# Kernel tuning notes

Measured on AMD Instinct MI355X. Metric: run time of the kernel, lower is better.

## Reference

```python
import jax, jax.numpy as jnp
import numpy as np

N_HEADS = 16
N_KV_HEADS = 4
HEAD_DIM = 128
D_MODEL = 2048
WINDOW = 1024
THETA = 10000.0
EPS = 1e-6


def _rmsnorm(x, w):
    var = jnp.mean(x * x, axis=-1, keepdims=True)
    return x * jax.lax.rsqrt(var + EPS) * w


def _rope(x, pos):
    # x: [B, H, S, D]; rotate-half (llama-style) RoPE
    d2 = HEAD_DIM // 2
    inv_freq = 1.0 / (THETA ** (jnp.arange(0, HEAD_DIM, 2, dtype=jnp.float32) / HEAD_DIM))
    ang = pos[:, None].astype(jnp.float32) * inv_freq[None, :]  # [S, D/2]
    cos = jnp.cos(ang)[None, None]
    sin = jnp.sin(ang)[None, None]
    x1, x2 = x[..., :d2], x[..., d2:]
    return jnp.concatenate([x1 * cos - x2 * sin, x1 * sin + x2 * cos], axis=-1)


def setup_inputs() -> dict:
    key = jax.random.key(0)
    ks = jax.random.split(key, 7)
    B, S = 1, 2048
    s = 0.02
    return {
        "x": jax.random.normal(ks[0], (B, S, D_MODEL), jnp.float32),
        "wq": jax.random.normal(ks[1], (N_HEADS * HEAD_DIM, D_MODEL), jnp.float32) * s,
        "wk": jax.random.normal(ks[2], (N_KV_HEADS * HEAD_DIM, D_MODEL), jnp.float32) * s,
        "wv": jax.random.normal(ks[3], (N_KV_HEADS * HEAD_DIM, D_MODEL), jnp.float32) * s,
        "wo": jax.random.normal(ks[4], (D_MODEL, N_HEADS * HEAD_DIM), jnp.float32) * s,
        "q_norm_w": jnp.ones((HEAD_DIM,), jnp.float32),
        "k_norm_w": jnp.ones((HEAD_DIM,), jnp.float32),
    }


def reference(x, wq, wk, wv, wo, q_norm_w, k_norm_w):
    B, S, _ = x.shape
    past_length = 0
    scale = HEAD_DIM ** -0.5
    n_rep = N_HEADS // N_KV_HEADS

    q = (x @ wq.T).reshape(B, S, N_HEADS, HEAD_DIM).transpose(0, 2, 1, 3)
    k = (x @ wk.T).reshape(B, S, N_KV_HEADS, HEAD_DIM).transpose(0, 2, 1, 3)
    v = (x @ wv.T).reshape(B, S, N_KV_HEADS, HEAD_DIM).transpose(0, 2, 1, 3)

    q = _rmsnorm(q, q_norm_w)
    k = _rmsnorm(k, k_norm_w)

    pos = jnp.arange(S) + past_length
    q = _rope(q, pos)
    k = _rope(k, pos)

    # GQA: materialize repeated KV heads, as in _repeat_kv
    k_rep = jnp.repeat(k, n_rep, axis=1)  # [B, H, S, D]
    v_rep = jnp.repeat(v, n_rep, axis=1)

    # sliding-window causal mask (total_seq_len=S > WINDOW)
    q_idx = jnp.arange(S)[:, None] + past_length
    k_idx = jnp.arange(S)[None, :]
    mask = (q_idx >= k_idx) & (q_idx - k_idx < WINDOW)  # [S, S]

    scores = jnp.einsum("bhqd,bhkd->bhqk", q, k_rep) * scale
    scores = jnp.where(mask[None, None], scores, jnp.float32(-jnp.inf))
    attn = jax.nn.softmax(scores, axis=-1)
    out = jnp.einsum("bhqk,bhkd->bhqd", attn, v_rep)

    out = out.transpose(0, 2, 1, 3).reshape(B, S, N_HEADS * HEAD_DIM)
    return out @ wo.T
```

## Files before the change

kernel.cpp:

```cpp
#include <hip/hip_runtime.h>
#include <hip/hip_bf16.h>
#include <cstdint>
#include <cstddef>

typedef __attribute__((ext_vector_type(4))) float f32x4;
typedef __attribute__((ext_vector_type(8))) short bf16x8;
typedef __attribute__((ext_vector_type(8))) unsigned short us8;

#define MFMA16(a, b, c) __builtin_amdgcn_mfma_f32_16x16x32_bf16(a, b, c, 0, 0, 0)

__device__ inline unsigned short f2bf(float f) {
    unsigned int u = __float_as_uint(f);
    u += 0x7fffu + ((u >> 16) & 1u);
    return (unsigned short)(u >> 16);
}
__device__ inline float bf2f(unsigned short u) {
    return __uint_as_float((unsigned int)u << 16);
}
__device__ inline unsigned short f2bf_fast(float f) {
    float r;
    asm("v_cvt_pk_bf16_f32 %0, %1, %2" : "=v"(r) : "v"(f), "v"(f));
    return (unsigned short)__float_as_uint(r);
}

__device__ inline void gload_lds16(const void* g, void* l) {
    __builtin_amdgcn_global_load_lds(
        (const __attribute__((address_space(1))) void*)g,
        (__attribute__((address_space(3))) void*)l, 16, 0, 0);
}
__device__ inline unsigned lds_addr(const void* p) {
    return (unsigned)(size_t)((__attribute__((address_space(3))) const void*)p);
}

__global__ __launch_bounds__(256) void prep_all(const float* __restrict__ x,
                                                const float* __restrict__ wq,
                                                const float* __restrict__ wk,
                                                const float* __restrict__ wv,
                                                const float* __restrict__ wo,
                                                unsigned short* __restrict__ xb,
                                                unsigned short* __restrict__ wqkv,
                                                unsigned short* __restrict__ wob,
                                                float2* __restrict__ tbl) {
    const int b = blockIdx.x;
    if (b < 14336) {
        const float* src; unsigned short* dst; int off4;
        if (b < 4096)       { src = x;  dst = xb;                 off4 = b; }
        else if (b < 8192)  { src = wq; dst = wqkv;               off4 = b - 4096; }
        else if (b < 9216)  { src = wk; dst = wqkv + 2048 * 2048; off4 = b - 8192; }
        else if (b < 10240) { src = wv; dst = wqkv + 2560 * 2048; off4 = b - 9216; }
        else                { src = wo; dst = wob;                off4 = b - 10240; }
        int i = (off4 * 256 + threadIdx.x) * 4;
        float4 v = *(const float4*)(src + i);
        ushort4 o;
        o.x = f2bf(v.x); o.y = f2bf(v.y); o.z = f2bf(v.z); o.w = f2bf(v.w);
        *(ushort4*)(dst + i) = o;
    } else {
        int idx = (b - 14336) * 256 + threadIdx.x;
        int row = idx >> 6, t = idx & 63;
        float inv_freq = exp2f((float)t * (-2.0f / 128.0f) * 13.287712379549449f);
        float s, c;
        sincosf((float)row * inv_freq, &s, &c);
        tbl[idx] = make_float2(c, s);
    }
}

__global__ __launch_bounds__(512, 2) void gemm256(const unsigned short* __restrict__ A,
                                                  const unsigned short* __restrict__ B,
                                                  unsigned short* __restrict__ Cp,
                                                  int M, int N, int Kfull, int kspan) {
    __shared__ unsigned short As[3][8192];
    __shared__ unsigned short Bs[3][8192];
    const int tid = threadIdx.x;
    const int lane = tid & 63, wave = tid >> 6;
    const int wr = wave >> 2, wc = wave & 3;
    const int l15 = lane & 15, l4 = lane >> 4;
    const int gx = gridDim.x;
    const int nwg = gx * gridDim.y;
    const int bid0 = blockIdx.y * gx + blockIdx.x;
    const int q8 = nwg >> 3, r8 = nwg & 7;
    const int xcd = bid0 & 7, sub = bid0 >> 3;
    const int wgid = ((xcd < r8) ? xcd * (q8 + 1) : r8 * (q8 + 1) + (xcd - r8) * q8) + sub;
    const int bm = wgid / gx, bn = wgid % gx;
    const int z = blockIdx.z;
    const unsigned short* Az = A + (size_t)z * kspan;
    const unsigned short* Bz = B + (size_t)z * kspan;
    unsigned short* C = Cp + (size_t)z * M * N;
    const int nK = kspan >> 5;

    f32x4 acc[8][4] = {};

    const int r0 = tid >> 2, qs = tid & 3;
    const int qsw = qs ^ ((r0 >> 1) & 3);
    const unsigned short* pa0 = Az + (size_t)(bm * 256 + r0) * Kfull + qsw * 8;
    const unsigned short* pa1 = pa0 + (size_t)128 * Kfull;
    const unsigned short* pb0 = Bz + (size_t)(bn * 256 + r0) * Kfull + qsw * 8;
    const unsigned short* pb1 = pb0 + (size_t)128 * Kfull;

#define STG(kt, bb)                                            \
    do {                                                       \
        gload_lds16(pa0 + (kt) * 32, &As[bb][tid * 8]);        \
        gload_lds16(pa1 + (kt) * 32, &As[bb][4096 + tid * 8]); \
        gload_lds16(pb0 + (kt) * 32, &Bs[bb][tid * 8]);        \
        gload_lds16(pb1 + (kt) * 32, &Bs[bb][4096 + tid * 8]); \
    } while (0)

    const int q = l4 ^ ((l15 >> 1) & 3);
    const unsigned aB = lds_addr(&As[0][0]) + (unsigned)((wr * 128 + l15) * 64 + q * 16);
    const unsigned bB = lds_addr(&Bs[0][0]) + (unsigned)((wc * 64 + l15) * 64 + q * 16);

#define DSR(dst, addr, off) \
    asm volatile("ds_read_b128 %0, %1 offset:" #off : "=v"(dst) : "v"(addr))

    STG(0, 0);
    STG(1, 1);
    int bc = 0, bs = 2;
    for (int kt = 0; kt < nK; ++kt) {
        if (kt + 1 < nK)
            asm volatile("s_waitcnt vmcnt(4)\ns_barrier" ::: "memory");
        else
            asm volatile("s_waitcnt vmcnt(0)\ns_barrier" ::: "memory");
        __builtin_amdgcn_sched_barrier(0);

        bf16x8 a[8], b[4];
        {
            const unsigned aA = aB + bc * 16384;
            const unsigned bA = bB + bc * 16384;
            DSR(a[0], aA, 0);    DSR(a[1], aA, 1024);
            DSR(a[2], aA, 2048); DSR(a[3], aA, 3072);
            DSR(a[4], aA, 4096); DSR(a[5], aA, 5120);
            DSR(a[6], aA, 6144); DSR(a[7], aA, 7168);
            DSR(b[0], bA, 0);    DSR(b[1], bA, 1024);
            DSR(b[2], bA, 2048); DSR(b[3], bA, 3072);
        }
        if (kt + 2 < nK) STG(kt + 2, bs);
        asm volatile("s_waitcnt lgkmcnt(0)" ::: "memory");
        __builtin_amdgcn_sched_barrier(0);

        __builtin_amdgcn_s_setprio(1);
#pragma unroll
        for (int m = 0; m < 8; ++m)
#pragma unroll
            for (int n = 0; n < 4; ++n)
                acc[m][n] = MFMA16(a[m], b[n], acc[m][n]);
        __builtin_amdgcn_s_setprio(0);

        if (++bc == 3) bc = 0;
        if (++bs == 3) bs = 0;
    }
#undef STG
#undef DSR

    for (int m = 0; m < 8; ++m)
        for (int n = 0; n < 4; ++n)
            for (int j = 0; j < 4; ++j) {
                int row = bm * 256 + wr * 128 + m * 16 + l4 * 4 + j;
                int col = bn * 256 + wc * 64 + n * 16 + l15;
                C[(size_t)row * N + col] = f2bf_fast(acc[m][n][j]);
            }
}

__global__ __launch_bounds__(256) void norm_rope(const unsigned short* __restrict__ p0,
                                                 const unsigned short* __restrict__ p1,
                                                 const float* __restrict__ qw,
                                                 const float* __restrict__ kw,
                                                 const float2* __restrict__ tbl,
                                                 unsigned short* __restrict__ Qb,
                                                 unsigned short* __restrict__ Kb) {
    const int row = blockIdx.x;
    const int head = blockIdx.y * 4 + (threadIdx.x >> 6);
    const int t = threadIdx.x & 63;
    const size_t off = (size_t)row * 3072 + head * 128;
    float x1 = bf2f(p0[off + t]) + bf2f(p1[off + t]);
    float x2 = bf2f(p0[off + t + 64]) + bf2f(p1[off + t + 64]);
    float ss = x1 * x1 + x2 * x2;
    for (int m = 32; m; m >>= 1) ss += __shfl_xor(ss, m);
    float r = rsqrtf(ss * (1.0f / 128.0f) + 1e-6f);
    const float* w = (head < 16) ? qw : kw;
    float y1 = x1 * r * w[t], y2 = x2 * r * w[t + 64];
    float2 cs = tbl[row * 64 + t];
    x1 = y1 * cs.x - y2 * cs.y;
    x2 = y1 * cs.y + y2 * cs.x;
    if (head < 16) {
        const float SCALE2 = 0.12751879526654698f;
        x1 *= SCALE2; x2 *= SCALE2;
    }
    unsigned short* dst = (head < 16) ? Qb + ((size_t)head * 2048 + row) * 128
                                      : Kb + ((size_t)(head - 16) * 2048 + row) * 128;
    dst[t] = f2bf(x1);
    dst[t + 64] = f2bf(x2);
}

__global__ __launch_bounds__(256) void transpose_v(const unsigned short* __restrict__ p0,
                                                   const unsigned short* __restrict__ p1,
                                                   unsigned short* __restrict__ VbT) {
    const int kt = blockIdx.x;
    const int h  = blockIdx.y;
    __shared__ unsigned short T[64 * 132];
    const int tid = threadIdx.x;
    for (int i = 0; i < 8; ++i) {
        int s = i * 256 + tid;
        int r = s >> 5, c = (s & 31) * 4;
        size_t off = (size_t)(kt * 64 + r) * 3072 + (20 + h) * 128 + c;
        ushort4 a = *(const ushort4*)(p0 + off);
        ushort4 b = *(const ushort4*)(p1 + off);
        ushort4 o;
        o.x = f2bf(bf2f(a.x) + bf2f(b.x));
        o.y = f2bf(bf2f(a.y) + bf2f(b.y));
        o.z = f2bf(bf2f(a.z) + bf2f(b.z));
        o.w = f2bf(bf2f(a.w) + bf2f(b.w));
        *(ushort4*)&T[r * 132 + c] = o;
    }
    __syncthreads();
    for (int i = 0; i < 4; ++i) {
        int s = i * 256 + tid;
        int d = s >> 3, ck = (s & 7) * 8;
        us8 v;
        for (int j = 0; j < 8; ++j) v[j] = T[(ck + j) * 132 + d];
        *(us8*)(VbT + (size_t)h * 128 * 2048 + (size_t)d * 2048 + kt * 64 + ck) = v;
    }
}

__global__ __launch_bounds__(256) void attn_fwd(const unsigned short* __restrict__ Qb,
                                                const unsigned short* __restrict__ Kb,
                                                const unsigned short* __restrict__ VbT,
                                                unsigned short* __restrict__ Ob) {
    const int bid = blockIdx.x;
    const int seq = bid >> 3;
    const int h = (bid & 7) * 2 + (seq >> 5);
    const int qt = seq & 31;
    const int kvh = h >> 2;
    const int q0 = qt * 64;
    __shared__ unsigned short Ks[2][64 * 128];
    __shared__ unsigned short Vs[128 * 64];
    __shared__ unsigned short Ps[4][16 * 72];
    const int tid = threadIdx.x;
    const int lane = tid & 63, wave = tid >> 6;
    const int l15 = lane & 15, l4 = lane >> 4;

    bf16x8 qf[4];
    {
        const unsigned short* qrow =
            Qb + ((size_t)h * 2048 + q0 + wave * 16 + l15) * 128 + l4 * 8;
        for (int kk = 0; kk < 4; ++kk) qf[kk] = *(const bf16x8*)(qrow + kk * 32);
    }
    f32x4 o[8] = {};
    float m2[4], lp[4];
    for (int j = 0; j < 4; ++j) { m2[j] = -1e30f; lp[j] = 0.0f; }
    const int kt_lo = (qt >= 16) ? (qt - 16) : 0;

    const unsigned short* Kh = Kb + (size_t)kvh * 2048 * 128;
    const unsigned short* Vh = VbT + (size_t)kvh * 128 * 2048;

    int ksr[4], ksc[4], vsr[4], vsc[4];
    for (int i = 0; i < 4; ++i) {
        int s = i * 256 + tid;
        ksr[i] = s >> 4;
        ksc[i] = (((s & 15) * 16) ^ ((ksr[i] & 7) << 4)) >> 1;
        vsr[i] = s >> 3;
        vsc[i] = (((s & 7) * 16) ^ ((vsr[i] & 7) << 4)) >> 1;
    }

    for (int i = 0; i < 4; ++i)
        gload_lds16(Kh + (size_t)(kt_lo * 64 + ksr[i]) * 128 + ksc[i], &Ks[0][(i * 256 + tid) * 8]);

    int cur = 0;
    for (int kt = kt_lo; kt <= qt; ++kt) {
        asm volatile("s_waitcnt vmcnt(0)\ns_barrier" ::: "memory");
        __builtin_amdgcn_sched_barrier(0);

        for (int i = 0; i < 4; ++i)
            gload_lds16(Vh + (size_t)vsr[i] * 2048 + kt * 64 + vsc[i], &Vs[(i * 256 + tid) * 8]);
        if (kt < qt) {
            for (int i = 0; i < 4; ++i)
                gload_lds16(Kh + (size_t)((kt + 1) * 64 + ksr[i]) * 128 + ksc[i],
                            &Ks[cur ^ 1][(i * 256 + tid) * 8]);
        }

        f32x4 s[4] = {};
        __builtin_amdgcn_s_setprio(1);
        for (int nn = 0; nn < 4; ++nn)
            for (int kk = 0; kk < 4; ++kk) {
                int r = nn * 16 + l15;
                int cb = (kk * 64 + l4 * 16) ^ ((r & 7) << 4);
                bf16x8 kf = *(const bf16x8*)((const char*)&Ks[cur][0] + r * 256 + cb);
                s[nn] = MFMA16(qf[kk], kf, s[nn]);
            }
        __builtin_amdgcn_s_setprio(0);

        float p[4][4];
        const bool masked = (kt == qt) || (qt >= 16 && kt == kt_lo);
        if (masked) {
            for (int nn = 0; nn < 4; ++nn) {
                int kc = kt * 64 + nn * 16 + l15;
                for (int j = 0; j < 4; ++j) {
                    int qr = q0 + wave * 16 + l4 * 4 + j;
                    unsigned diff = (unsigned)(qr - kc);
                    p[nn][j] = (diff < 1024u) ? s[nn][j] : -1e30f;
                }
            }
        } else {
            for (int nn = 0; nn < 4; ++nn)
                for (int j = 0; j < 4; ++j) p[nn][j] = s[nn][j];
        }

        float mxl[4];
        bool flag = true;
        for (int j = 0; j < 4; ++j) {
            mxl[j] = fmaxf(fmaxf(p[0][j], p[1][j]), fmaxf(p[2][j], p[3][j]));
            flag = flag && (mxl[j] <= m2[j] + 11.0f);
        }
        if (!__all(flag)) {
            for (int j = 0; j < 4; ++j) {
                float mx = mxl[j];
                for (int mk = 8; mk; mk >>= 1) mx = fmaxf(mx, __shfl_xor(mx, mk));
                float mnew = fmaxf(m2[j], mx);
                float corr = exp2f(m2[j] - mnew);
                m2[j] = mnew;
                lp[j] *= corr;
                for (int dd = 0; dd < 8; ++dd) o[dd][j] *= corr;
            }
        }
        for (int j = 0; j < 4; ++j) {
            float rs = 0.0f;
            for (int nn = 0; nn < 4; ++nn) {
                float pv = exp2f(p[nn][j] - m2[j]);
                p[nn][j] = pv;
                rs += pv;
            }
            lp[j] += rs;
        }

        for (int j = 0; j < 4; ++j)
            for (int nn = 0; nn < 4; ++nn)
                Ps[wave][(l4 * 4 + j) * 72 + nn * 16 + l15] = f2bf_fast(p[nn][j]);

        bf16x8 pa[2];
        for (int kk2 = 0; kk2 < 2; ++kk2)
            pa[kk2] = *(const bf16x8*)&Ps[wave][l15 * 72 + kk2 * 32 + l4 * 8];

        if (kt < qt)
            asm volatile("s_waitcnt vmcnt(4)\ns_barrier" ::: "memory");
        else
            asm volatile("s_waitcnt vmcnt(0)\ns_barrier" ::: "memory");
        __builtin_amdgcn_sched_barrier(0);

        __builtin_amdgcn_s_setprio(1);
        for (int dd = 0; dd < 8; ++dd)
            for (int kk2 = 0; kk2 < 2; ++kk2) {
                int d = dd * 16 + l15;
                int cb = (kk2 * 64 + l4 * 16) ^ ((d & 7) << 4);
                bf16x8 vf = *(const bf16x8*)((const char*)&Vs[0] + d * 128 + cb);
                o[dd] = MFMA16(pa[kk2], vf, o[dd]);
            }
        __builtin_amdgcn_s_setprio(0);
        cur ^= 1;
    }

    for (int j = 0; j < 4; ++j) {
        float lt = lp[j];
        for (int mk = 8; mk; mk >>= 1) lt += __shfl_xor(lt, mk);
        float inv = 1.0f / lt;
        int row = q0 + wave * 16 + l4 * 4 + j;
        unsigned short* orow = Ob + (size_t)row * 2048 + h * 128;
        for (int dd = 0; dd < 8; ++dd) orow[dd * 16 + l15] = f2bf_fast(o[dd][j] * inv);
    }
}

__global__ __launch_bounds__(256) void add4(const unsigned short* __restrict__ p,
                                            float* __restrict__ out, int n) {
    int i = (blockIdx.x * 256 + threadIdx.x) * 8;
    if (i >= n) return;
    us8 a = *(const us8*)(p + i);
    us8 b = *(const us8*)(p + 4194304 + i);
    us8 c = *(const us8*)(p + 8388608 + i);
    us8 d = *(const us8*)(p + 12582912 + i);
    f32x4 o0, o1;
    for (int j = 0; j < 4; ++j)
        o0[j] = (bf2f(a[j]) + bf2f(b[j])) + (bf2f(c[j]) + bf2f(d[j]));
    for (int j = 0; j < 4; ++j)
        o1[j] = (bf2f(a[j + 4]) + bf2f(b[j + 4])) + (bf2f(c[j + 4]) + bf2f(d[j + 4]));
    *(f32x4*)(out + i) = o0;
    *(f32x4*)(out + i + 4) = o1;
}

extern "C" void kernel_launch(void* const* d_in, const int* in_sizes, int n_in,
                              void* d_out, int out_size, void* d_ws, size_t ws_size,
                              hipStream_t stream) {
    const float* x  = (const float*)d_in[0];
    const float* wq = (const float*)d_in[1];
    const float* wk = (const float*)d_in[2];
    const float* wv = (const float*)d_in[3];
    const float* wo = (const float*)d_in[4];
    const float* wo_ = wo; (void)wo_;
    const float* qw = (const float*)d_in[5];
    const float* kw = (const float*)d_in[6];
    float* out = (float*)d_out;

    char* ws = (char*)d_ws;
    unsigned short* xb   = (unsigned short*)(ws + 0);
    unsigned short* wqkv = (unsigned short*)(ws + 8388608);
    unsigned short* wob  = (unsigned short*)(ws + 20971520);
    unsigned short* qkvP = (unsigned short*)(ws + 29360128);
    unsigned short* Qb   = (unsigned short*)(ws + 54525952);
    unsigned short* Kb   = (unsigned short*)(ws + 62914560);
    unsigned short* VbT  = (unsigned short*)(ws + 65011712);
    unsigned short* Ob   = (unsigned short*)(ws + 67108864);
    unsigned short* outP = (unsigned short*)(ws + 29360128);
    float2*         tbl  = (float2*)(ws + 104857600);

    prep_all<<<dim3(14848), dim3(256), 0, stream>>>(x, wq, wk, wv, wo, xb, wqkv, wob, tbl);
    gemm256<<<dim3(12, 8, 2), dim3(512), 0, stream>>>(xb, wqkv, qkvP, 2048, 3072, 2048, 1024);
    norm_rope<<<dim3(2048, 5), dim3(256), 0, stream>>>(qkvP, qkvP + 2048 * 3072, qw, kw, tbl, Qb, Kb);
    transpose_v<<<dim3(32, 4), dim3(256), 0, stream>>>(qkvP, qkvP + 2048 * 3072, VbT);
    attn_fwd<<<dim3(512), dim3(256), 0, stream>>>(Qb, Kb, VbT, Ob);
    gemm256<<<dim3(8, 8, 4), dim3(512), 0, stream>>>(Ob, wob, outP, 2048, 2048, 2048, 512);
    add4<<<dim3(2048), dim3(256), 0, stream>>>(outP, out, 2048 * 2048);
}
```

Before: 133.7 us.

## Share K/V tiles across two query heads per attention block

The attention kernel now launches 256 blocks of 512 threads. Each block covers two query heads that map to the same KV head, so each K/V tile loaded into LDS serves twice as many waves, halving global K/V traffic and per-head load instructions. The P tile is written as packed bf16 pairs into an XOR-swizzled LDS layout to reduce bank conflicts. To keep the P·V product correct, the V transpose kernel stores keys in a matching permuted order. Larger blocks reduce the number of resident blocks and leave the causal load imbalance between blocks unchanged.

Measured after the change: 126.5 us. -5.4%, faster.

```diff
diff --git a/kernel.cpp b/kernel.cpp
--- a/kernel.cpp
+++ b/kernel.cpp
@@ -215,32 +215,37 @@
         int s = i * 256 + tid;
         int d = s >> 3, ck = (s & 7) * 8;
         us8 v;
-        for (int j = 0; j < 8; ++j) v[j] = T[(ck + j) * 132 + d];
+        for (int j = 0; j < 8; ++j) {
+            int c = ck + j;
+            int k = (c & 3) * 16 + (c >> 2);
+            v[j] = T[k * 132 + d];
+        }
         *(us8*)(VbT + (size_t)h * 128 * 2048 + (size_t)d * 2048 + kt * 64 + ck) = v;
     }
 }
 
-__global__ __launch_bounds__(256) void attn_fwd(const unsigned short* __restrict__ Qb,
+__global__ __launch_bounds__(512) void attn_fwd(const unsigned short* __restrict__ Qb,
                                                 const unsigned short* __restrict__ Kb,
                                                 const unsigned short* __restrict__ VbT,
                                                 unsigned short* __restrict__ Ob) {
     const int bid = blockIdx.x;
-    const int seq = bid >> 3;
-    const int h = (bid & 7) * 2 + (seq >> 5);
-    const int qt = seq & 31;
-    const int kvh = h >> 2;
+    const int p = bid & 7;
+    const int qt = bid >> 3;
     const int q0 = qt * 64;
     __shared__ unsigned short Ks[2][64 * 128];
     __shared__ unsigned short Vs[128 * 64];
-    __shared__ unsigned short Ps[4][16 * 72];
+    __shared__ unsigned short Ps[8][16 * 68];
     const int tid = threadIdx.x;
     const int lane = tid & 63, wave = tid >> 6;
     const int l15 = lane & 15, l4 = lane >> 4;
+    const int h = 2 * p + (wave >> 2);
+    const int rgrp = wave & 3;
+    const int kvh = p >> 1;
 
     bf16x8 qf[4];
     {
         const unsigned short* qrow =
-            Qb + ((size_t)h * 2048 + q0 + wave * 16 + l15) * 128 + l4 * 8;
+            Qb + ((size_t)h * 2048 + q0 + rgrp * 16 + l15) * 128 + l4 * 8;
         for (int kk = 0; kk < 4; ++kk) qf[kk] = *(const bf16x8*)(qrow + kk * 32);
     }
     f32x4 o[8] = {};
@@ -251,29 +256,31 @@
     const unsigned short* Kh = Kb + (size_t)kvh * 2048 * 128;
     const unsigned short* Vh = VbT + (size_t)kvh * 128 * 2048;
 
-    int ksr[4], ksc[4], vsr[4], vsc[4];
-    for (int i = 0; i < 4; ++i) {
-        int s = i * 256 + tid;
+    int ksr[2], ksc[2], vsr[2], vsc[2];
+    for (int i = 0; i < 2; ++i) {
+        int s = i * 512 + tid;
         ksr[i] = s >> 4;
         ksc[i] = (((s & 15) * 16) ^ ((ksr[i] & 7) << 4)) >> 1;
         vsr[i] = s >> 3;
         vsc[i] = (((s & 7) * 16) ^ ((vsr[i] & 7) << 4)) >> 1;
     }
 
-    for (int i = 0; i < 4; ++i)
-        gload_lds16(Kh + (size_t)(kt_lo * 64 + ksr[i]) * 128 + ksc[i], &Ks[0][(i * 256 + tid) * 8]);
+    for (int i = 0; i < 2; ++i)
+        gload_lds16(Kh + (size_t)(kt_lo * 64 + ksr[i]) * 128 + ksc[i],
+                    &Ks[0][(i * 512 + tid) * 8]);
 
     int cur = 0;
     for (int kt = kt_lo; kt <= qt; ++kt) {
         asm volatile("s_waitcnt vmcnt(0)\ns_barrier" ::: "memory");
         __builtin_amdgcn_sched_barrier(0);
 
-        for (int i = 0; i < 4; ++i)
-            gload_lds16(Vh + (size_t)vsr[i] * 2048 + kt * 64 + vsc[i], &Vs[(i * 256 + tid) * 8]);
+        for (int i = 0; i < 2; ++i)
+            gload_lds16(Vh + (size_t)vsr[i] * 2048 + kt * 64 + vsc[i],
+                        &Vs[(i * 512 + tid) * 8]);
         if (kt < qt) {
-            for (int i = 0; i < 4; ++i)
+            for (int i = 0; i < 2; ++i)
                 gload_lds16(Kh + (size_t)((kt + 1) * 64 + ksr[i]) * 128 + ksc[i],
-                            &Ks[cur ^ 1][(i * 256 + tid) * 8]);
+                            &Ks[cur ^ 1][(i * 512 + tid) * 8]);
         }
 
         f32x4 s[4] = {};
@@ -287,26 +294,26 @@
             }
         __builtin_amdgcn_s_setprio(0);
 
-        float p[4][4];
+        float pv4[4][4];
         const bool masked = (kt == qt) || (qt >= 16 && kt == kt_lo);
         if (masked) {
             for (int nn = 0; nn < 4; ++nn) {
                 int kc = kt * 64 + nn * 16 + l15;
                 for (int j = 0; j < 4; ++j) {
-                    int qr = q0 + wave * 16 + l4 * 4 + j;
+                    int qr = q0 + rgrp * 16 + l4 * 4 + j;
                     unsigned diff = (unsigned)(qr - kc);
-                    p[nn][j] = (diff < 1024u) ? s[nn][j] : -1e30f;
+                    pv4[nn][j] = (diff < 1024u) ? s[nn][j] : -1e30f;
                 }
             }
         } else {
             for (int nn = 0; nn < 4; ++nn)
-                for (int j = 0; j < 4; ++j) p[nn][j] = s[nn][j];
+                for (int j = 0; j < 4; ++j) pv4[nn][j] = s[nn][j];
         }
 
         float mxl[4];
         bool flag = true;
         for (int j = 0; j < 4; ++j) {
-            mxl[j] = fmaxf(fmaxf(p[0][j], p[1][j]), fmaxf(p[2][j], p[3][j]));
+            mxl[j] = fmaxf(fmaxf(pv4[0][j], pv4[1][j]), fmaxf(pv4[2][j], pv4[3][j]));
             flag = flag && (mxl[j] <= m2[j] + 11.0f);
         }
         if (!__all(flag)) {
@@ -323,23 +330,30 @@
         for (int j = 0; j < 4; ++j) {
             float rs = 0.0f;
             for (int nn = 0; nn < 4; ++nn) {
-                float pv = exp2f(p[nn][j] - m2[j]);
-                p[nn][j] = pv;
+                float pv = exp2f(pv4[nn][j] - m2[j]);
+                pv4[nn][j] = pv;
                 rs += pv;
             }
             lp[j] += rs;
         }
 
-        for (int j = 0; j < 4; ++j)
-            for (int nn = 0; nn < 4; ++nn)
-                Ps[wave][(l4 * 4 + j) * 72 + nn * 16 + l15] = f2bf_fast(p[nn][j]);
+        for (int j = 0; j < 4; ++j) {
+            int row = l4 * 4 + j;
+            unsigned lo, hi;
+            asm("v_cvt_pk_bf16_f32 %0, %1, %2" : "=v"(lo) : "v"(pv4[0][j]), "v"(pv4[1][j]));
+            asm("v_cvt_pk_bf16_f32 %0, %1, %2" : "=v"(hi) : "v"(pv4[2][j]), "v"(pv4[3][j]));
+            int cb = (l15 * 8) ^ ((row & 7) << 4);
+            *(uint2*)((char*)&Ps[wave][0] + row * 136 + cb) = make_uint2(lo, hi);
+        }
 
         bf16x8 pa[2];
-        for (int kk2 = 0; kk2 < 2; ++kk2)
-            pa[kk2] = *(const bf16x8*)&Ps[wave][l15 * 72 + kk2 * 32 + l4 * 8];
+        for (int kk2 = 0; kk2 < 2; ++kk2) {
+            int cb = (kk2 * 64 + l4 * 16) ^ ((l15 & 7) << 4);
+            pa[kk2] = *(const bf16x8*)((const char*)&Ps[wave][0] + l15 * 136 + cb);
+        }
 
         if (kt < qt)
-            asm volatile("s_waitcnt vmcnt(4)\ns_barrier" ::: "memory");
+            asm volatile("s_waitcnt vmcnt(2)\ns_barrier" ::: "memory");
         else
             asm volatile("s_waitcnt vmcnt(0)\ns_barrier" ::: "memory");
         __builtin_amdgcn_sched_barrier(0);
@@ -360,7 +374,7 @@
         float lt = lp[j];
         for (int mk = 8; mk; mk >>= 1) lt += __shfl_xor(lt, mk);
         float inv = 1.0f / lt;
-        int row = q0 + wave * 16 + l4 * 4 + j;
+        int row = q0 + rgrp * 16 + l4 * 4 + j;
         unsigned short* orow = Ob + (size_t)row * 2048 + h * 128;
         for (int dd = 0; dd < 8; ++dd) orow[dd * 16 + l15] = f2bf_fast(o[dd][j] * inv);
     }
@@ -391,7 +405,6 @@
     const float* wk = (const float*)d_in[2];
     const float* wv = (const float*)d_in[3];
     const float* wo = (const float*)d_in[4];
-    const float* wo_ = wo; (void)wo_;
     const float* qw = (const float*)d_in[5];
     const float* kw = (const float*)d_in[6];
     float* out = (float*)d_out;
@@ -412,7 +425,7 @@
     gemm256<<<dim3(12, 8, 2), dim3(512), 0, stream>>>(xb, wqkv, qkvP, 2048, 3072, 2048, 1024);
     norm_rope<<<dim3(2048, 5), dim3(256), 0, stream>>>(qkvP, qkvP + 2048 * 3072, qw, kw, tbl, Qb, Kb);
     transpose_v<<<dim3(32, 4), dim3(256), 0, stream>>>(qkvP, qkvP + 2048 * 3072, VbT);
-    attn_fwd<<<dim3(512), dim3(256), 0, stream>>>(Qb, Kb, VbT, Ob);
+    attn_fwd<<<dim3(256), dim3(512), 0, stream>>>(Qb, Kb, VbT, Ob);
     gemm256<<<dim3(8, 8, 4), dim3(512), 0, stream>>>(Ob, wob, outP, 2048, 2048, 2048, 512);
     add4<<<dim3(2048), dim3(256), 0, stream>>>(outP, out, 2048 * 2048);
 }
```
